# Kernel tuning notes

Measured on AMD Instinct MI355X. Metric: run time of the kernel, lower is better.

## Reference

```python
import jax, jax.numpy as jnp
import numpy as np


def eops_2_to_2(x):
    # x: (N, D, m, m) -> (N, D, 15, m, m), Maron et al. equivariant basis with 'inf' normalization
    m = x.shape[-1]
    fm = float(m)
    eye = jnp.eye(m, dtype=x.dtype)
    diag = jnp.diagonal(x, axis1=-2, axis2=-1)          # (N, D, m)
    sum_diag = diag.sum(-1, keepdims=True)              # (N, D, 1)
    sum_rows = x.sum(-1)                                # (N, D, m) sum over columns j
    sum_cols = x.sum(-2)                                # (N, D, m) sum over rows i
    tot = x.sum((-2, -1))                               # (N, D)

    de = lambda v: v[..., :, None] * eye                # diag_embed (N,D,m) -> (N,D,m,m)
    b_row = lambda v: jnp.broadcast_to(v[..., :, None], v.shape + (m,))           # row i constant = v[i]
    b_col = lambda v: jnp.broadcast_to(v[..., None, :], v.shape[:-1] + (m, m))    # col j constant = v[j]

    op1 = de(diag)
    op2 = de(jnp.broadcast_to(sum_diag, diag.shape)) / fm
    op3 = de(sum_rows) / fm
    op4 = de(sum_cols) / fm
    op5 = de(jnp.broadcast_to(tot[..., None], diag.shape)) / (fm * fm)
    op6 = b_row(sum_cols) / fm
    op7 = b_row(sum_rows) / fm
    op8 = b_col(sum_cols) / fm
    op9 = b_col(sum_rows) / fm
    op10 = x
    op11 = jnp.swapaxes(x, -1, -2)
    op12 = b_row(diag)
    op13 = b_col(diag)
    op14 = jnp.broadcast_to(sum_diag[..., None], x.shape) / fm
    op15 = jnp.broadcast_to(tot[..., None, None], x.shape) / (fm * fm)
    return jnp.stack([op1, op2, op3, op4, op5, op6, op7, op8,
                      op9, op10, op11, op12, op13, op14, op15], axis=2)


def setup_inputs() -> dict:
    key = jax.random.key(0)
    k1, k2 = jax.random.split(key)
    N, D, S, B, m = 32, 32, 32, 15, 128
    std = np.sqrt(2.0 / (D + S + B)).astype(np.float32)
    inputs = jax.random.normal(k1, (N, D, m, m), dtype=jnp.float32)
    coefs = jax.random.normal(k2, (D, S, B), dtype=jnp.float32) * std
    bias = jnp.zeros((1, S, 1, 1), dtype=jnp.float32)
    diag_bias = jnp.zeros((1, S, 1, 1), dtype=jnp.float32)
    return {"inputs": inputs, "coefs": coefs, "bias": bias, "diag_bias": diag_bias}


def reference(inputs, coefs, bias, diag_bias):
    ops = eops_2_to_2(inputs)                               # (N, D, 15, m, m)
    out = jnp.einsum('dsb,ndbij->nsij', coefs, ops)         # (N, S, m, m)
    m = out.shape[-1]
    eye = jnp.eye(m, dtype=out.dtype)[None, None]           # (1,1,m,m)
    return out + bias + eye * diag_bias
```

## Files before the change

kernel.cpp:

```cpp
#include <hip/hip_runtime.h>

#define N_ 32
#define D_ 32
#define S_ 32
#define M_ 128
#define MM_ (M_ * M_)
#define INV_M (1.0f / 128.0f)
#define INV_M2 (1.0f / (128.0f * 128.0f))

typedef float f32x4 __attribute__((ext_vector_type(4)));
typedef __bf16 bf16x8 __attribute__((ext_vector_type(8)));

#define WS_ROWSUM  0
#define WS_COLSUM  131072
#define WS_DIAG    262144
#define WS_SUMDIAG 393216
#define WS_TOT     394240
#define WS_RV      395264
#define WS_CV      526336
#define WS_DG      657408
#define WS_WBF16   788480

__device__ __forceinline__ unsigned short f2bf(float f) {
    unsigned u = __float_as_uint(f);
    u += 0x7fffu + ((u >> 16) & 1u);
    return (unsigned short)(u >> 16);
}

__global__ __launch_bounds__(256) void eq2_reduce(const float* __restrict__ x,
                                                  float* __restrict__ ws) {
    int nd = blockIdx.x;
    int t  = threadIdx.x;
    int g  = t >> 5;
    int j4 = t & 31;

    const float4* xp = (const float4*)(x + (size_t)nd * MM_);

    float* rowsum  = ws + WS_ROWSUM;
    float* colsum  = ws + WS_COLSUM;
    float* diag    = ws + WS_DIAG;
    float* sumdiag = ws + WS_SUMDIAG;
    float* tot     = ws + WS_TOT;

    float4 cs = {0.f, 0.f, 0.f, 0.f};
    float dsum = 0.f, ttot = 0.f;

    for (int r = 0; r < 16; ++r) {
        int i = g * 16 + r;
        float4 v = xp[i * 32 + j4];
        cs.x += v.x; cs.y += v.y; cs.z += v.z; cs.w += v.w;
        float rp = v.x + v.y + v.z + v.w;
        ttot += rp;
        int c = i - 4 * j4;
        if (c >= 0 && c < 4) {
            float dv = (c == 0) ? v.x : (c == 1) ? v.y : (c == 2) ? v.z : v.w;
            diag[nd * M_ + i] = dv;
            dsum += dv;
        }
        float rs = rp;
        for (int msk = 1; msk < 32; msk <<= 1) rs += __shfl_xor(rs, msk, 64);
        if ((t & 31) == 0) rowsum[nd * M_ + i] = rs;
    }

    __shared__ float4 cs_lds[8][32];
    __shared__ float  red[2][4];
    cs_lds[g][j4] = cs;

    for (int msk = 1; msk < 64; msk <<= 1) {
        dsum += __shfl_xor(dsum, msk, 64);
        ttot += __shfl_xor(ttot, msk, 64);
    }
    int wave = t >> 6, lane = t & 63;
    if (lane == 0) { red[0][wave] = dsum; red[1][wave] = ttot; }
    __syncthreads();

    if (t < 32) {
        float4 a = cs_lds[0][t];
        for (int gg = 1; gg < 8; ++gg) {
            float4 b = cs_lds[gg][t];
            a.x += b.x; a.y += b.y; a.z += b.z; a.w += b.w;
        }
        ((float4*)(colsum + nd * M_))[t] = a;
    }
    if (t == 0) {
        sumdiag[nd] = red[0][0] + red[0][1] + red[0][2] + red[0][3];
        tot[nd]     = red[1][0] + red[1][1] + red[1][2] + red[1][3];
    }
}

__global__ __launch_bounds__(128) void eq2_combine(const float* __restrict__ coefs,
                                                   const float* __restrict__ bias,
                                                   const float* __restrict__ diag_bias,
                                                   float* __restrict__ ws) {
    int b = blockIdx.x;
    int n = b >> 5, s = b & 31;
    int i = threadIdx.x;

    const float* rowsum  = ws + WS_ROWSUM;
    const float* colsum  = ws + WS_COLSUM;
    const float* diag    = ws + WS_DIAG;
    const float* sumdiag = ws + WS_SUMDIAG;
    const float* tot     = ws + WS_TOT;

    float rv = 0.f, cv = 0.f, dg = 0.f, kk = 0.f;
    for (int d = 0; d < D_; ++d) {
        const float* cf = coefs + (d * S_ + s) * 15;
        float rs = rowsum[(n * D_ + d) * M_ + i];
        float c2 = colsum[(n * D_ + d) * M_ + i];
        float dv = diag[(n * D_ + d) * M_ + i];
        float sd = sumdiag[n * D_ + d];
        float tt = tot[n * D_ + d];
        rv += (cf[5] * c2 + cf[6] * rs) * INV_M + cf[11] * dv;
        cv += (cf[7] * c2 + cf[8] * rs) * INV_M + cf[12] * dv;
        dg += cf[0] * dv + (cf[1] * sd + cf[2] * rs + cf[3] * c2) * INV_M
              + cf[4] * tt * INV_M2;
        kk += cf[13] * sd * INV_M + cf[14] * tt * INV_M2;
    }
    ws[WS_RV + (n * S_ + s) * M_ + i] = rv + kk + bias[s];
    ws[WS_CV + (n * S_ + s) * M_ + i] = cv;
    ws[WS_DG + (n * S_ + s) * M_ + i] = dg + diag_bias[s];

    if (n == 0 && i < 32) {
        int d = i;
        unsigned short* wsbf = (unsigned short*)(ws + WS_WBF16);
        const float* cf = coefs + (d * S_ + s) * 15;
        wsbf[s * 40 + d]        = f2bf(cf[9]);
        wsbf[(32 + s) * 40 + d] = f2bf(cf[10]);
    }
}

__global__ __launch_bounds__(512, 4) void eq2_main(const float* __restrict__ x,
                                                   const float* __restrict__ ws_,
                                                   float* __restrict__ out) {
    const float* ws = (const float*)__builtin_assume_aligned(ws_, 256);
    int lid = blockIdx.x;
    int n   = (lid & 7) + 8 * (lid >> 8);
    int b   = (lid >> 3) & 31;

    int AR, AC, BR, BC, diagpair;
    if (b < 28) {
        int ti = 0, rem = b;
        while (rem >= 7 - ti) { rem -= 7 - ti; ++ti; }
        int tj = ti + 1 + rem;
        AR = ti * 16; AC = tj * 16;
        BR = tj * 16; BC = ti * 16;
        diagpair = 0;
    } else {
        int p = b - 28;
        AR = AC = (2 * p) * 16;
        BR = BC = (2 * p + 1) * 16;
        diagpair = 1;
    }

    int t    = threadIdx.x;
    int w    = t >> 6;
    int lane = t & 63;
    int lg   = lane >> 4;
    int lj   = lane & 15;

    __shared__ __align__(16) unsigned short XB[2][256][40];
    __shared__ float trf[8 * 545];
    __shared__ float lds_rv[S_][32];
    __shared__ float lds_cv[S_][32];
    __shared__ float lds_dg[S_][32];

    const unsigned short* wsbf = (const unsigned short*)(ws + WS_WBF16);
    const float* xn = x + (size_t)n * (D_ * MM_);

    bf16x8 A10[2], A11[2];
#pragma unroll
    for (int mt = 0; mt < 2; ++mt) {
        A10[mt] = *(const bf16x8*)(wsbf + (mt * 16 + lj) * 40 + lg * 8);
        A11[mt] = *(const bf16x8*)(wsbf + (32 + mt * 16 + lj) * 40 + lg * 8);
    }

    {
        const float* Rv = ws + WS_RV;
        const float* Cv = ws + WS_CV;
        const float* Dg = ws + WS_DG;
#pragma unroll
        for (int k = 0; k < 2; ++k) {
            int idx = k * 512 + t;
            int s = idx >> 5, q = idx & 31;
            int base = (n * S_ + s) * M_;
            int ro = (q < 16) ? AR + q : BR + (q - 16);
            int co = (q < 16) ? AC + q : BC + (q - 16);
            lds_rv[s][q] = Rv[base + ro];
            lds_cv[s][q] = Cv[base + co];
            if (diagpair) lds_dg[s][q] = Dg[base + ro];
        }
    }

    {
        int h  = t >> 8;
        int ip = (t >> 4) & 15;
        int jp = t & 15;
#pragma unroll
        for (int tt = 0; tt < 2; ++tt) {
            int R = tt ? BR : AR, C = tt ? BC : AC;
            float v[16];
#pragma unroll
            for (int rep = 0; rep < 16; ++rep)
                v[rep] = xn[(size_t)(h * 16 + rep) * MM_ + (R + ip) * M_ + C + jp];
            unsigned u[8];
#pragma unroll
            for (int k2 = 0; k2 < 8; ++k2)
                u[k2] = (unsigned)f2bf(v[2 * k2]) | ((unsigned)f2bf(v[2 * k2 + 1]) << 16);
            unsigned short* dst = &XB[tt][ip * 16 + jp][h * 16];
            uint4 u0; u0.x = u[0]; u0.y = u[1]; u0.z = u[2]; u0.w = u[3];
            uint4 u1; u1.x = u[4]; u1.y = u[5]; u1.z = u[6]; u1.w = u[7];
            ((uint4*)dst)[0] = u0;
            ((uint4*)dst)[1] = u1;
        }
    }

    __syncthreads();

    f32x4 aY[4][2], aZ[4][2];
#pragma unroll
    for (int k = 0; k < 4; ++k)
#pragma unroll
        for (int mt = 0; mt < 2; ++mt) { aY[k][mt] = 0.f; aZ[k][mt] = 0.f; }

#pragma unroll
    for (int k = 0; k < 4; ++k) {
        int nt = w * 4 + k;
        int tt = nt >> 4, il = nt & 15;
        bf16x8 Bf = *(const bf16x8*)(&XB[tt][il * 16 + lj][lg * 8]);
        aY[k][0] = __builtin_amdgcn_mfma_f32_16x16x32_bf16(A10[0], Bf, aY[k][0], 0, 0, 0);
        aY[k][1] = __builtin_amdgcn_mfma_f32_16x16x32_bf16(A10[1], Bf, aY[k][1], 0, 0, 0);
        aZ[k][0] = __builtin_amdgcn_mfma_f32_16x16x32_bf16(A11[0], Bf, aZ[k][0], 0, 0, 0);
        aZ[k][1] = __builtin_amdgcn_mfma_f32_16x16x32_bf16(A11[1], Bf, aZ[k][1], 0, 0, 0);
    }

#pragma unroll
    for (int r = 0; r < 4; ++r) {
        if (r) __syncthreads();
#pragma unroll
        for (int k = 0; k < 4; ++k) {
            int nt = w * 4 + k;
            int tt = nt >> 4, il = nt & 15;
#pragma unroll
            for (int mt = 0; mt < 2; ++mt)
                trf[(mt * 4 + lg) * 545 + tt * 272 + il * 17 + lj] = aZ[k][mt][r];
        }
        __syncthreads();
#pragma unroll
        for (int k = 0; k < 4; ++k) {
            int nt = w * 4 + k;
            int tt = nt >> 4, il = nt & 15;
            int ttp = diagpair ? tt : 1 - tt;
            int Rt = tt ? BR : AR, Ct = tt ? BC : AC;
#pragma unroll
            for (int mt = 0; mt < 2; ++mt) {
                int s = mt * 16 + 4 * lg + r;
                float zt = trf[(mt * 4 + lg) * 545 + ttp * 272 + lj * 17 + il];
                float o = aY[k][mt][r] + zt + lds_rv[s][tt * 16 + il] + lds_cv[s][tt * 16 + lj];
                if (diagpair && il == lj) o += lds_dg[s][tt * 16 + il];
                out[(size_t)(n * S_ + s) * MM_ + (Rt + il) * M_ + Ct + lj] = o;
            }
        }
    }
}

extern "C" void kernel_launch(void* const* d_in, const int* in_sizes, int n_in,
                              void* d_out, int out_size, void* d_ws, size_t ws_size,
                              hipStream_t stream) {
    const float* x         = (const float*)d_in[0];
    const float* coefs     = (const float*)d_in[1];
    const float* bias      = (const float*)d_in[2];
    const float* diag_bias = (const float*)d_in[3];
    float* out = (float*)d_out;
    float* ws  = (float*)d_ws;

    hipLaunchKernelGGL(eq2_reduce,  dim3(N_ * D_), dim3(256), 0, stream, x, ws);
    hipLaunchKernelGGL(eq2_combine, dim3(N_ * S_), dim3(128), 0, stream, coefs, bias, diag_bias, ws);
    hipLaunchKernelGGL(eq2_main,    dim3(1024), dim3(512), 0, stream, x, ws, out);
}
```

Measured before the change: 53.47 us.

## Precompute bf16 channel-transposed input in prep pass and feed MFMA from it

Replaces the per-(n,d) reduction kernel with a prep kernel that reads x once, computes row, column and diagonal partial sums, and also writes a bf16 copy of x laid out as [n][i][j][d] in workspace. A small fold kernel then combines the column-sum, diag-sum and total partials. The main kernel loads its MFMA B fragments straight from this transposed bf16 buffer instead of re-reading fp32 x with strided D accesses and staging through LDS. In exchange there is an extra kernel launch, a 32 MB bf16 write and read round trip through workspace, and heavier register use in the prep kernel.

```diff
diff --git a/kernel.cpp b/kernel.cpp
--- a/kernel.cpp
+++ b/kernel.cpp
@@ -20,6 +20,10 @@
 #define WS_CV      526336
 #define WS_DG      657408
 #define WS_WBF16   788480
+#define WS_CSP     789760
+#define WS_SDP     1838336
+#define WS_TOTP    1846528
+#define WS_XT      1854720
 
 __device__ __forceinline__ unsigned short f2bf(float f) {
     unsigned u = __float_as_uint(f);
@@ -27,64 +31,125 @@
     return (unsigned short)(u >> 16);
 }
 
-__global__ __launch_bounds__(256) void eq2_reduce(const float* __restrict__ x,
-                                                  float* __restrict__ ws) {
-    int nd = blockIdx.x;
-    int t  = threadIdx.x;
-    int g  = t >> 5;
-    int j4 = t & 31;
-
-    const float4* xp = (const float4*)(x + (size_t)nd * MM_);
-
-    float* rowsum  = ws + WS_ROWSUM;
-    float* colsum  = ws + WS_COLSUM;
-    float* diag    = ws + WS_DIAG;
-    float* sumdiag = ws + WS_SUMDIAG;
-    float* tot     = ws + WS_TOT;
-
-    float4 cs = {0.f, 0.f, 0.f, 0.f};
-    float dsum = 0.f, ttot = 0.f;
-
-    for (int r = 0; r < 16; ++r) {
-        int i = g * 16 + r;
-        float4 v = xp[i * 32 + j4];
-        cs.x += v.x; cs.y += v.y; cs.z += v.z; cs.w += v.w;
-        float rp = v.x + v.y + v.z + v.w;
-        ttot += rp;
-        int c = i - 4 * j4;
-        if (c >= 0 && c < 4) {
-            float dv = (c == 0) ? v.x : (c == 1) ? v.y : (c == 2) ? v.z : v.w;
-            diag[nd * M_ + i] = dv;
-            dsum += dv;
-        }
-        float rs = rp;
-        for (int msk = 1; msk < 32; msk <<= 1) rs += __shfl_xor(rs, msk, 64);
-        if ((t & 31) == 0) rowsum[nd * M_ + i] = rs;
-    }
-
-    __shared__ float4 cs_lds[8][32];
-    __shared__ float  red[2][4];
-    cs_lds[g][j4] = cs;
-
-    for (int msk = 1; msk < 64; msk <<= 1) {
-        dsum += __shfl_xor(dsum, msk, 64);
-        ttot += __shfl_xor(ttot, msk, 64);
-    }
-    int wave = t >> 6, lane = t & 63;
-    if (lane == 0) { red[0][wave] = dsum; red[1][wave] = ttot; }
+__global__ __launch_bounds__(512, 2) void eq2_prep(const float* __restrict__ x,
+                                                   float* __restrict__ ws) {
+    int blk = blockIdx.x;
+    int n   = (blk & 7) + 8 * (blk >> 6);
+    int rg  = (blk >> 3) & 7;
+    int R0  = rg * 16;
+
+    int t    = threadIdx.x;
+    int jj   = t & 127;
+    int q    = t >> 7;
+    int lane = t & 63;
+    int w    = t >> 6;
+
+    const float* xn = x + (size_t)n * (D_ * MM_);
+    unsigned short* xt = (unsigned short*)(ws + WS_XT) + (size_t)n * 16384 * 32;
+
+    __shared__ float lds_row[16][32][2];
+    __shared__ float lds_diag[16][32];
+    __shared__ float lds_cs[4][8][128];
+
+    float cacc[32];
+#pragma unroll
+    for (int d = 0; d < 32; ++d) cacc[d] = 0.f;
+
+    for (int c = 0; c < 4; ++c) {
+        int li = 4 * c + q;
+        int gi = R0 + li;
+        const float* src = xn + gi * M_ + jj;
+
+        float v[32];
+#pragma unroll
+        for (int d = 0; d < 32; ++d) v[d] = src[(size_t)d * MM_];
+
+        {
+            unsigned u[16];
+#pragma unroll
+            for (int k = 0; k < 16; ++k)
+                u[k] = (unsigned)f2bf(v[2 * k]) | ((unsigned)f2bf(v[2 * k + 1]) << 16);
+            uint4* dst = (uint4*)(xt + (size_t)(gi * 128 + jj) * 32);
+            uint4 a = {u[0], u[1], u[2], u[3]};
+            uint4 b = {u[4], u[5], u[6], u[7]};
+            uint4 cc = {u[8], u[9], u[10], u[11]};
+            uint4 dd = {u[12], u[13], u[14], u[15]};
+            dst[0] = a; dst[1] = b; dst[2] = cc; dst[3] = dd;
+        }
+
+#pragma unroll
+        for (int d = 0; d < 32; ++d) cacc[d] += v[d];
+
+#pragma unroll
+        for (int d = 0; d < 32; ++d) {
+            float r = v[d];
+            for (int msk = 1; msk < 64; msk <<= 1) r += __shfl_xor(r, msk, 64);
+            if (lane == 0) lds_row[li][d][w & 1] = r;
+        }
+
+        if (jj == gi) {
+            float* diag = ws + WS_DIAG;
+#pragma unroll
+            for (int d = 0; d < 32; ++d) {
+                diag[(n * D_ + d) * M_ + gi] = v[d];
+                lds_diag[li][d] = v[d];
+            }
+        }
+    }
     __syncthreads();
 
+    {
+        int li = t >> 5, d = t & 31;
+        float rsum = lds_row[li][d][0] + lds_row[li][d][1];
+        (ws + WS_ROWSUM)[(n * D_ + d) * M_ + R0 + li] = rsum;
+    }
     if (t < 32) {
-        float4 a = cs_lds[0][t];
-        for (int gg = 1; gg < 8; ++gg) {
-            float4 b = cs_lds[gg][t];
-            a.x += b.x; a.y += b.y; a.z += b.z; a.w += b.w;
-        }
-        ((float4*)(colsum + nd * M_))[t] = a;
-    }
-    if (t == 0) {
-        sumdiag[nd] = red[0][0] + red[0][1] + red[0][2] + red[0][3];
-        tot[nd]     = red[1][0] + red[1][1] + red[1][2] + red[1][3];
+        int d = t;
+        float tp = 0.f, sp = 0.f;
+        for (int li = 0; li < 16; ++li) {
+            tp += lds_row[li][d][0] + lds_row[li][d][1];
+            sp += lds_diag[li][d];
+        }
+        (ws + WS_TOTP)[(n * 8 + rg) * 32 + d] = tp;
+        (ws + WS_SDP)[(n * 8 + rg) * 32 + d] = sp;
+    }
+
+    for (int g = 0; g < 4; ++g) {
+        __syncthreads();
+#pragma unroll
+        for (int k = 0; k < 8; ++k) lds_cs[q][k][jj] = cacc[g * 8 + k];
+        __syncthreads();
+#pragma unroll
+        for (int r = 0; r < 2; ++r) {
+            int idx = t + 512 * r;
+            int d8 = idx >> 7, j2 = idx & 127;
+            float s = lds_cs[0][d8][j2] + lds_cs[1][d8][j2]
+                    + lds_cs[2][d8][j2] + lds_cs[3][d8][j2];
+            (ws + WS_CSP)[(size_t)((n * 8 + rg) * 32 + g * 8 + d8) * 128 + j2] = s;
+        }
+    }
+}
+
+__global__ __launch_bounds__(128) void eq2_foldcs(float* __restrict__ ws) {
+    int lid = blockIdx.x;
+    int n   = (lid & 7) + 8 * (lid >> 8);
+    int d   = (lid >> 3) & 31;
+    int j   = threadIdx.x;
+
+    const float* csp = ws + WS_CSP;
+    float s = 0.f;
+    for (int rg = 0; rg < 8; ++rg)
+        s += csp[(size_t)((n * 8 + rg) * 32 + d) * 128 + j];
+    (ws + WS_COLSUM)[(n * D_ + d) * M_ + j] = s;
+
+    if (j == 0) {
+        float sd = 0.f, tt = 0.f;
+        for (int rg = 0; rg < 8; ++rg) {
+            sd += (ws + WS_SDP)[(n * 8 + rg) * 32 + d];
+            tt += (ws + WS_TOTP)[(n * 8 + rg) * 32 + d];
+        }
+        (ws + WS_SUMDIAG)[n * D_ + d] = sd;
+        (ws + WS_TOT)[n * D_ + d]     = tt;
     }
 }
 
@@ -129,8 +194,7 @@
     }
 }
 
-__global__ __launch_bounds__(512, 4) void eq2_main(const float* __restrict__ x,
-                                                   const float* __restrict__ ws_,
+__global__ __launch_bounds__(512, 4) void eq2_main(const float* __restrict__ ws_,
                                                    float* __restrict__ out) {
     const float* ws = (const float*)__builtin_assume_aligned(ws_, 256);
     int lid = blockIdx.x;
@@ -158,14 +222,13 @@
     int lg   = lane >> 4;
     int lj   = lane & 15;
 
-    __shared__ __align__(16) unsigned short XB[2][256][40];
     __shared__ float trf[8 * 545];
     __shared__ float lds_rv[S_][32];
     __shared__ float lds_cv[S_][32];
     __shared__ float lds_dg[S_][32];
 
     const unsigned short* wsbf = (const unsigned short*)(ws + WS_WBF16);
-    const float* xn = x + (size_t)n * (D_ * MM_);
+    const unsigned short* xtn  = (const unsigned short*)(ws + WS_XT) + (size_t)n * 16384 * 32;
 
     bf16x8 A10[2], A11[2];
 #pragma unroll
@@ -191,46 +254,27 @@
         }
     }
 
-    {
-        int h  = t >> 8;
-        int ip = (t >> 4) & 15;
-        int jp = t & 15;
-#pragma unroll
-        for (int tt = 0; tt < 2; ++tt) {
-            int R = tt ? BR : AR, C = tt ? BC : AC;
-            float v[16];
-#pragma unroll
-            for (int rep = 0; rep < 16; ++rep)
-                v[rep] = xn[(size_t)(h * 16 + rep) * MM_ + (R + ip) * M_ + C + jp];
-            unsigned u[8];
-#pragma unroll
-            for (int k2 = 0; k2 < 8; ++k2)
-                u[k2] = (unsigned)f2bf(v[2 * k2]) | ((unsigned)f2bf(v[2 * k2 + 1]) << 16);
-            unsigned short* dst = &XB[tt][ip * 16 + jp][h * 16];
-            uint4 u0; u0.x = u[0]; u0.y = u[1]; u0.z = u[2]; u0.w = u[3];
-            uint4 u1; u1.x = u[4]; u1.y = u[5]; u1.z = u[6]; u1.w = u[7];
-            ((uint4*)dst)[0] = u0;
-            ((uint4*)dst)[1] = u1;
-        }
-    }
-
-    __syncthreads();
-
     f32x4 aY[4][2], aZ[4][2];
 #pragma unroll
     for (int k = 0; k < 4; ++k)
 #pragma unroll
         for (int mt = 0; mt < 2; ++mt) { aY[k][mt] = 0.f; aZ[k][mt] = 0.f; }
 
+    bf16x8 Bf[4];
 #pragma unroll
     for (int k = 0; k < 4; ++k) {
         int nt = w * 4 + k;
         int tt = nt >> 4, il = nt & 15;
-        bf16x8 Bf = *(const bf16x8*)(&XB[tt][il * 16 + lj][lg * 8]);
-        aY[k][0] = __builtin_amdgcn_mfma_f32_16x16x32_bf16(A10[0], Bf, aY[k][0], 0, 0, 0);
-        aY[k][1] = __builtin_amdgcn_mfma_f32_16x16x32_bf16(A10[1], Bf, aY[k][1], 0, 0, 0);
-        aZ[k][0] = __builtin_amdgcn_mfma_f32_16x16x32_bf16(A11[0], Bf, aZ[k][0], 0, 0, 0);
-        aZ[k][1] = __builtin_amdgcn_mfma_f32_16x16x32_bf16(A11[1], Bf, aZ[k][1], 0, 0, 0);
+        int Rt = tt ? BR : AR, Ct = tt ? BC : AC;
+        int pos = (Rt + il) * 128 + Ct + lj;
+        Bf[k] = *(const bf16x8*)(xtn + (size_t)pos * 32 + lg * 8);
+    }
+#pragma unroll
+    for (int k = 0; k < 4; ++k) {
+        aY[k][0] = __builtin_amdgcn_mfma_f32_16x16x32_bf16(A10[0], Bf[k], aY[k][0], 0, 0, 0);
+        aY[k][1] = __builtin_amdgcn_mfma_f32_16x16x32_bf16(A10[1], Bf[k], aY[k][1], 0, 0, 0);
+        aZ[k][0] = __builtin_amdgcn_mfma_f32_16x16x32_bf16(A11[0], Bf[k], aZ[k][0], 0, 0, 0);
+        aZ[k][1] = __builtin_amdgcn_mfma_f32_16x16x32_bf16(A11[1], Bf[k], aZ[k][1], 0, 0, 0);
     }
 
 #pragma unroll
@@ -273,7 +317,8 @@
     float* out = (float*)d_out;
     float* ws  = (float*)d_ws;
 
-    hipLaunchKernelGGL(eq2_reduce,  dim3(N_ * D_), dim3(256), 0, stream, x, ws);
+    hipLaunchKernelGGL(eq2_prep,    dim3(256),  dim3(512), 0, stream, x, ws);
+    hipLaunchKernelGGL(eq2_foldcs,  dim3(1024), dim3(128), 0, stream, ws);
     hipLaunchKernelGGL(eq2_combine, dim3(N_ * S_), dim3(128), 0, stream, coefs, bias, diag_bias, ws);
-    hipLaunchKernelGGL(eq2_main,    dim3(1024), dim3(512), 0, stream, x, ws, out);
-}
+    hipLaunchKernelGGL(eq2_main,    dim3(1024), dim3(512), 0, stream, ws, out);
+}
```

Measured after the change: 75.89 us. 41.9% more time.
